# Kernel tuning notes

Hardware: AMD Instinct MI355X
Metric: run time of the kernel (lower is better)

Reference implementation:

```python
import jax, jax.numpy as jnp
import numpy as np

N = 50000      # nodes
E = 600000     # edges (avg degree 12)
F_IN = 128     # num_features
H = 128        # hidden_feats (== F_IN so both conv layers share weight shapes)
C = 10         # num_classes
L = 2          # num_layers


def setup_inputs() -> dict:
    key = jax.random.key(0)
    ks = jax.random.split(key, 12)
    s = 0.05
    x = jax.random.normal(ks[0], (N, F_IN), dtype=jnp.float32)
    edge_index = jax.random.randint(ks[1], (2, E), 0, N, dtype=jnp.int64)
    # Stacked per-layer TransformerConv params (heads=1): query/key/value/skip linears.
    Wq = jax.random.normal(ks[2], (L, H, F_IN), dtype=jnp.float32) * s
    bq = jax.random.normal(ks[3], (L, H), dtype=jnp.float32) * s
    Wk = jax.random.normal(ks[4], (L, H, F_IN), dtype=jnp.float32) * s
    bk = jax.random.normal(ks[5], (L, H), dtype=jnp.float32) * s
    Wv = jax.random.normal(ks[6], (L, H, F_IN), dtype=jnp.float32) * s
    bv = jax.random.normal(ks[7], (L, H), dtype=jnp.float32) * s
    Ws = jax.random.normal(ks[8], (L, H, F_IN), dtype=jnp.float32) * s
    bs = jax.random.normal(ks[9], (L, H), dtype=jnp.float32) * s
    fc_W = jax.random.normal(ks[10], (C, H), dtype=jnp.float32) * s
    fc_b = jax.random.normal(ks[11], (C,), dtype=jnp.float32) * s
    return {"x": x, "edge_index": edge_index, "Wq": Wq, "bq": bq, "Wk": Wk,
            "bk": bk, "Wv": Wv, "bv": bv, "Ws": Ws, "bs": bs,
            "fc_W": fc_W, "fc_b": fc_b}


def _transformer_conv(h, src, dst, Wq, bq, Wk, bk, Wv, bv, Ws, bs):
    # PyG TransformerConv, heads=1, concat=True, root_weight=True, eval mode.
    d = Wq.shape[0]
    scale = 1.0 / np.sqrt(d).astype(np.float32)
    q = h @ Wq.T + bq          # [N, d]
    k = h @ Wk.T + bk          # [N, d]
    v = h @ Wv.T + bv          # [N, d]
    # per-edge attention score: <q_dst, k_src> / sqrt(d)
    scores = jnp.sum(q[dst] * k[src], axis=-1) * scale   # [E]
    # scatter-softmax over incoming edges of each destination node
    m = jax.ops.segment_max(scores, dst, num_segments=N)           # [N]
    e = jnp.exp(scores - m[dst])                                   # [E]
    denom = jax.ops.segment_sum(e, dst, num_segments=N)            # [N]
    alpha = e / denom[dst]                                         # [E]
    agg = jax.ops.segment_sum(alpha[:, None] * v[src], dst, num_segments=N)  # [N, d]
    return agg + (h @ Ws.T + bs)  # root/skip connection


def reference(x, edge_index, Wq, bq, Wk, bk, Wv, bv, Ws, bs, fc_W, fc_b):
    src = edge_index[0]
    dst = edge_index[1]
    h = x
    for l in range(L):  # fixed small layer loop
        h = _transformer_conv(h, src, dst, Wq[l], bq[l], Wk[l], bk[l],
                              Wv[l], bv[l], Ws[l], bs[l])
        h = jax.nn.relu(h)  # dropout is identity in eval mode
    logits = h @ fc_W.T + fc_b  # [N, C]
    return jax.nn.log_softmax(logits, axis=1)
```

## Files before the change

### kernel.cpp

```cpp
#include <hip/hip_runtime.h>
#include <math.h>

#define N_NODES 50000
#define N_EDGES 600000
#define DIM 128
#define NCLS 10
#define MTILES 391
#define CHUNKS_PER_TILE 2048
#define NB_SCAN 49

typedef _Float16 h2 __attribute__((ext_vector_type(2)));
typedef _Float16 half8 __attribute__((ext_vector_type(8)));
typedef __attribute__((ext_vector_type(4))) float f32x4;
typedef unsigned char uchar;

__device__ inline h2 pkh(float a, float b) {
    auto r = __builtin_amdgcn_cvt_pkrtz(a, b);
    return *(h2*)&r;
}
__device__ inline unsigned h2u(h2 v) { return *(unsigned*)&v; }
__device__ inline h2 u2h(unsigned u) { return *(h2*)&u; }

__device__ inline float dot2acc(h2 a, h2 b, float c) {
#if __has_builtin(__builtin_amdgcn_fdot2)
    return __builtin_amdgcn_fdot2(a, b, c, false);
#else
    return fmaf((float)a.x, (float)b.x, fmaf((float)a.y, (float)b.y, c));
#endif
}

__device__ inline h2 dec2lo(unsigned w) {
    return u2h(__builtin_amdgcn_perm(0u, w, 0x010C000Cu));
}
__device__ inline h2 dec2hi(unsigned w) {
    return u2h(__builtin_amdgcn_perm(0u, w, 0x030C020Cu));
}
__device__ inline unsigned rnd8(h2 v) {
    unsigned u = h2u(v);
    return u + 0x007F007Fu + ((u >> 8) & 0x00010001u);
}

__global__ void deg_kernel(const int* __restrict__ dst, int* __restrict__ deg) {
    int e = blockIdx.x * blockDim.x + threadIdx.x;
    if (e < N_EDGES) atomicAdd(&deg[dst[e]], 1);
}

__global__ __launch_bounds__(1024) void scan1_kernel(
        const int* __restrict__ deg, int* __restrict__ row_start,
        int* __restrict__ partials) {
    __shared__ int buf[1024];
    int b = blockIdx.x, t = threadIdx.x;
    int i = b * 1024 + t;
    buf[t] = (i < N_NODES) ? deg[i] : 0;
    __syncthreads();
    for (int off = 1; off < 1024; off <<= 1) {
        int tv = (t >= off) ? buf[t - off] : 0;
        __syncthreads();
        buf[t] += tv;
        __syncthreads();
    }
    if (i < N_NODES) row_start[i + 1] = buf[t];
    if (t == 1023) partials[b] = buf[1023];
}

__global__ __launch_bounds__(1024) void scan3_kernel(
        const int* __restrict__ partials, int* __restrict__ row_start,
        int* __restrict__ cursor, int* __restrict__ col) {
    __shared__ int boff_s;
    int b = blockIdx.x, t = threadIdx.x;
    if (t < 64) {
        int v = (t < b) ? partials[t] : 0;
        #pragma unroll
        for (int off = 32; off >= 1; off >>= 1) v += __shfl_xor(v, off);
        if (t == 0) boff_s = v;
    }
    __syncthreads();
    int boff = boff_s;
    int i = b * 1024 + t;
    if (i < N_NODES) {
        int val = row_start[i + 1] + boff;
        row_start[i + 1] = val;
        if (i + 1 < N_NODES) cursor[i + 1] = val;
    }
    if (i == 0) { row_start[0] = 0; cursor[0] = 0; }
    if (b == 0 && t < 16) col[N_EDGES + t] = 0;
}

__global__ void fill_kernel(const int* __restrict__ src, const int* __restrict__ dst,
                            int* __restrict__ cursor, int* __restrict__ col) {
    int e = blockIdx.x * blockDim.x + threadIdx.x;
    if (e < N_EDGES) {
        int pos = atomicAdd(&cursor[dst[e]], 1);
        col[pos] = src[e];
    }
}

__global__ __launch_bounds__(256) void convertw_kernel(
        const float* __restrict__ Wq, const float* __restrict__ Wk,
        const float* __restrict__ Wv, const float* __restrict__ Ws,
        unsigned short* __restrict__ wfrag) {
    int b = blockIdx.x;
    int l = b >> 2, m = b & 3;
    const float* W = (m == 0 ? Wq : m == 1 ? Wk : m == 2 ? Wv : Ws) + l * DIM * DIM;
    unsigned short* out = wfrag + (size_t)b * (CHUNKS_PER_TILE * 8);
    for (int i = threadIdx.x; i < CHUNKS_PER_TILE; i += 256) {
        int tile = i >> 6, lane = i & 63;
        int row = (tile >> 2) * 16 + (lane & 15);
        int k0 = (tile & 3) * 32 + (lane >> 4) * 8;
        const float4* p = (const float4*)(W + row * DIM + k0);
        float4 a = p[0], bb = p[1];
        uint4 o;
        o.x = h2u(pkh(a.x, a.y));  o.y = h2u(pkh(a.z, a.w));
        o.z = h2u(pkh(bb.x, bb.y)); o.w = h2u(pkh(bb.z, bb.w));
        *(uint4*)(out + (size_t)i * 8) = o;
    }
}

template <bool F32IN>
__global__ __launch_bounds__(512) void linear_kernel(
        const void* __restrict__ hb_,
        const unsigned short* __restrict__ wfrag,
        const float* __restrict__ bq, const float* __restrict__ bk,
        const float* __restrict__ bv, const float* __restrict__ bs,
        unsigned short* __restrict__ Qb, uchar* __restrict__ K8,
        uchar* __restrict__ V8, unsigned short* __restrict__ Sb) {
    __shared__ unsigned short hs[16384];
    __shared__ unsigned short wsm[16384];
    int tid = threadIdx.x;
    int tile = blockIdx.x;
    uint4* lh = (uint4*)hs;
    uint4* lw = (uint4*)wsm;
    #pragma unroll
    for (int j = 0; j < 4; ++j) {
        int i = tid + j * 512;
        int s = i >> 6, lane = i & 63;
        int row = tile * 128 + ((s >> 2) << 4) + (lane & 15);
        int k0 = ((s & 3) << 5) + ((lane >> 4) << 3);
        row = row < N_NODES ? row : N_NODES - 1;
        if (F32IN) {
            const float* hf = (const float*)hb_;
            const float4* p = (const float4*)(hf + (size_t)row * DIM + k0);
            float4 a = p[0], bb = p[1];
            uint4 o;
            o.x = h2u(pkh(a.x, a.y));  o.y = h2u(pkh(a.z, a.w));
            o.z = h2u(pkh(bb.x, bb.y)); o.w = h2u(pkh(bb.z, bb.w));
            lh[i] = o;
        } else {
            const unsigned short* hh = (const unsigned short*)hb_;
            lh[i] = *(const uint4*)(hh + (size_t)row * DIM + k0);
        }
    }
    int wave = tid >> 6, lane = tid & 63;
    int node = tile * 128 + wave * 16 + (lane & 15);
    int cq = (lane >> 4) * 4;

    #pragma unroll
    for (int m = 0; m < 4; ++m) {
        const uint4* gw = (const uint4*)(wfrag + (size_t)m * (CHUNKS_PER_TILE * 8));
        __syncthreads();
        #pragma unroll
        for (int j = 0; j < 4; ++j) lw[tid + j * 512] = gw[tid + j * 512];
        __syncthreads();

        f32x4 acc[8];
        #pragma unroll
        for (int nt = 0; nt < 8; ++nt) acc[nt] = (f32x4){0.f, 0.f, 0.f, 0.f};
        #pragma unroll
        for (int ks = 0; ks < 4; ++ks) {
            half8 hbv = *(const half8*)(lh + (wave * 4 + ks) * 64 + lane);
            #pragma unroll
            for (int nt = 0; nt < 8; ++nt)
                acc[nt] = __builtin_amdgcn_mfma_f32_16x16x32_f16(
                              *(const half8*)(lw + (nt * 4 + ks) * 64 + lane),
                              hbv, acc[nt], 0, 0, 0);
        }

        const float* bias = (m == 0 ? bq : m == 1 ? bk : m == 2 ? bv : bs);
        if (node < N_NODES) {
            if (m == 0 || m == 3) {
                unsigned short* ob = (m == 0) ? Qb : Sb;
                #pragma unroll
                for (int nt = 0; nt < 8; ++nt) {
                    int colv = nt * 16 + cq;
                    float4 bi = *(const float4*)(bias + colv);
                    uint2 o;
                    o.x = h2u(pkh(acc[nt][0] + bi.x, acc[nt][1] + bi.y));
                    o.y = h2u(pkh(acc[nt][2] + bi.z, acc[nt][3] + bi.w));
                    *(uint2*)(ob + (size_t)node * DIM + colv) = o;
                }
            } else {
                uchar* ob = ((m == 1) ? K8 : V8) + (size_t)node * DIM;
                #pragma unroll
                for (int nt = 0; nt < 8; ++nt) {
                    int colv = nt * 16 + cq;
                    float4 bi = *(const float4*)(bias + colv);
                    unsigned uA = rnd8(pkh(acc[nt][0] + bi.x, acc[nt][1] + bi.y));
                    unsigned uB = rnd8(pkh(acc[nt][2] + bi.z, acc[nt][3] + bi.w));
                    *(unsigned*)(ob + colv) =
                        __builtin_amdgcn_perm(uB, uA, 0x07050301u);
                }
            }
        }
    }
}

template <bool LOGITS>
__global__ __launch_bounds__(256, 4) void attn_kernel(
        const unsigned short* __restrict__ Qb, const uchar* __restrict__ K8,
        const uchar* __restrict__ V8, const unsigned short* __restrict__ Sb,
        const int* __restrict__ row_start, const int* __restrict__ col,
        unsigned short* __restrict__ hout, float* __restrict__ outF,
        const float* __restrict__ fcW, const float* __restrict__ fcb) {
    int wave = threadIdx.x >> 6;
    int lane = threadIdx.x & 63;
    int g = lane >> 4, gl = lane & 15;
    int n = blockIdx.x * 4 + wave;
    if (n >= N_NODES) return;

    const uchar* Kc = K8 + (gl << 3);
    const uchar* Vc = V8 + (gl << 3);
    const float qsf = 0.08838834764831843f * 1.4426950408889634f;
    h2 qsv = pkh(qsf, qsf);
    uint4 qu = *(const uint4*)((const char*)Qb + (((unsigned)n) << 8) + (gl << 4));
    h2 q0 = u2h(qu.x) * qsv, q1 = u2h(qu.y) * qsv;
    h2 q2 = u2h(qu.z) * qsv, q3 = u2h(qu.w) * qsv;

    int e0 = row_start[n], e1 = row_start[n + 1];
    int deg = e1 - e0;
    const float NEG = -1.0e30f;
    float den = 0.f;
    h2 a0 = (h2)0, a1 = (h2)0, a2 = (h2)0, a3 = (h2)0;

#define LOAD4(eb_, k_, v_)                                                  \
    do {                                                                     \
        unsigned o0 = ((unsigned)col[(eb_)]) << 7;                           \
        unsigned o1 = ((unsigned)col[(eb_) + 4]) << 7;                       \
        unsigned o2 = ((unsigned)col[(eb_) + 8]) << 7;                       \
        unsigned o3 = ((unsigned)col[(eb_) + 12]) << 7;                      \
        k_[0] = *(const uint2*)(Kc + o0); v_[0] = *(const uint2*)(Vc + o0);  \
        k_[1] = *(const uint2*)(Kc + o1); v_[1] = *(const uint2*)(Vc + o1);  \
        k_[2] = *(const uint2*)(Kc + o2); v_[2] = *(const uint2*)(Vc + o2);  \
        k_[3] = *(const uint2*)(Kc + o3); v_[3] = *(const uint2*)(Vc + o3);  \
    } while (0)

#define EDOT(ku_) ({                                                         \
        float p_ = dot2acc(dec2lo((ku_).x), q0, 0.f);                        \
        p_ = dot2acc(dec2hi((ku_).x), q1, p_);                               \
        p_ = dot2acc(dec2lo((ku_).y), q2, p_);                               \
        p_ = dot2acc(dec2hi((ku_).y), q3, p_);                               \
        p_ += __shfl_xor(p_, 1); p_ += __shfl_xor(p_, 2);                    \
        p_ += __shfl_xor(p_, 4); p_ += __shfl_xor(p_, 8);                    \
        p_; })

#define ACCE(w_, vu_)                                                        \
    do {                                                                     \
        h2 w2 = pkh(w_, w_);                                                 \
        a0 = a0 + w2 * dec2lo((vu_).x);                                      \
        a1 = a1 + w2 * dec2hi((vu_).x);                                      \
        a2 = a2 + w2 * dec2lo((vu_).y);                                      \
        a3 = a3 + w2 * dec2hi((vu_).y);                                      \
    } while (0)

#define COMPUTE4(eb_, k_, v_)                                                \
    do {                                                                     \
        float p0 = EDOT(k_[0]), p1 = EDOT(k_[1]);                            \
        float p2 = EDOT(k_[2]), p3 = EDOT(k_[3]);                            \
        p0 = (eb_) < e1      ? p0 : NEG;                                     \
        p1 = (eb_) + 4 < e1  ? p1 : NEG;                                     \
        p2 = (eb_) + 8 < e1  ? p2 : NEG;                                     \
        p3 = (eb_) + 12 < e1 ? p3 : NEG;                                     \
        float w0 = exp2f(p0), w1 = exp2f(p1);                                \
        float w2_ = exp2f(p2), w3 = exp2f(p3);                               \
        den += (w0 + w1) + (w2_ + w3);                                       \
        ACCE(w0, v_[0]); ACCE(w1, v_[1]);                                    \
        ACCE(w2_, v_[2]); ACCE(w3, v_[3]);                                   \
    } while (0)

    if (deg > 0) {
        int B = (deg + 15) >> 4;
        int eb = e0 + g;
        uint2 k[4], v[4];
        LOAD4(eb, k, v);
        for (int b = 0;;) {
            uint2 nk[4], nv[4];
            bool more = (b + 1 < B);
            if (more) LOAD4(eb + 16, nk, nv);
            COMPUTE4(eb, k, v);
            if (!more) break;
            ++b; eb += 16;
            #pragma unroll
            for (int i = 0; i < 4; ++i) { k[i] = nk[i]; v[i] = nv[i]; }
        }
    }
#undef LOAD4
#undef EDOT
#undef ACCE
#undef COMPUTE4

    float d = den;
    d += __shfl_xor(d, 16);
    d += __shfl_xor(d, 32);
    a0 = a0 + u2h((unsigned)__shfl_xor((int)h2u(a0), 16));
    a0 = a0 + u2h((unsigned)__shfl_xor((int)h2u(a0), 32));
    a1 = a1 + u2h((unsigned)__shfl_xor((int)h2u(a1), 16));
    a1 = a1 + u2h((unsigned)__shfl_xor((int)h2u(a1), 32));
    a2 = a2 + u2h((unsigned)__shfl_xor((int)h2u(a2), 16));
    a2 = a2 + u2h((unsigned)__shfl_xor((int)h2u(a2), 32));
    a3 = a3 + u2h((unsigned)__shfl_xor((int)h2u(a3), 16));
    a3 = a3 + u2h((unsigned)__shfl_xor((int)h2u(a3), 32));
    float inv = (d > 0.f) ? 1.f / d : 0.f;

    uint4 su = *(const uint4*)((const char*)Sb + (((unsigned)n) << 8) + (gl << 4));
    h2 s0 = u2h(su.x), s1 = u2h(su.y), s2 = u2h(su.z), s3 = u2h(su.w);
    float o0 = fmaxf(fmaf((float)a0.x, inv, (float)s0.x), 0.f);
    float o1 = fmaxf(fmaf((float)a0.y, inv, (float)s0.y), 0.f);
    float o2 = fmaxf(fmaf((float)a1.x, inv, (float)s1.x), 0.f);
    float o3 = fmaxf(fmaf((float)a1.y, inv, (float)s1.y), 0.f);
    float o4 = fmaxf(fmaf((float)a2.x, inv, (float)s2.x), 0.f);
    float o5 = fmaxf(fmaf((float)a2.y, inv, (float)s2.y), 0.f);
    float o6 = fmaxf(fmaf((float)a3.x, inv, (float)s3.x), 0.f);
    float o7 = fmaxf(fmaf((float)a3.y, inv, (float)s3.y), 0.f);

    if (!LOGITS) {
        if (g == 0) {
            uint4 o;
            o.x = h2u(pkh(o0, o1)); o.y = h2u(pkh(o2, o3));
            o.z = h2u(pkh(o4, o5)); o.w = h2u(pkh(o6, o7));
            *(uint4*)((char*)hout + (((unsigned)n) << 8) + (gl << 4)) = o;
        }
    } else {
        float lg[NCLS];
        #pragma unroll
        for (int c = 0; c < NCLS; ++c) {
            const float4* fw = (const float4*)(fcW + c * DIM + gl * 8);
            float4 wa = fw[0], wb = fw[1];
            float pc = o0 * wa.x + o1 * wa.y + o2 * wa.z + o3 * wa.w
                     + o4 * wb.x + o5 * wb.y + o6 * wb.z + o7 * wb.w;
            pc += __shfl_xor(pc, 1); pc += __shfl_xor(pc, 2);
            pc += __shfl_xor(pc, 4); pc += __shfl_xor(pc, 8);
            lg[c] = pc + fcb[c];
        }
        float mx = lg[0];
        #pragma unroll
        for (int c = 1; c < NCLS; ++c) mx = fmaxf(mx, lg[c]);
        float se = 0.f;
        #pragma unroll
        for (int c = 0; c < NCLS; ++c) se += __expf(lg[c] - mx);
        float lse = mx + logf(se);
        if (g == 0 && gl < NCLS) {
            float myv = 0.f;
            #pragma unroll
            for (int c = 0; c < NCLS; ++c) if (gl == c) myv = lg[c];
            outF[(size_t)n * NCLS + gl] = myv - lse;
        }
    }
}

extern "C" void kernel_launch(void* const* d_in, const int* in_sizes, int n_in,
                              void* d_out, int out_size, void* d_ws, size_t ws_size,
                              hipStream_t stream) {
    const float* x   = (const float*)d_in[0];
    const int*   ei  = (const int*)d_in[1];
    const float* Wq  = (const float*)d_in[2];
    const float* bq  = (const float*)d_in[3];
    const float* Wk  = (const float*)d_in[4];
    const float* bk  = (const float*)d_in[5];
    const float* Wv  = (const float*)d_in[6];
    const float* bv  = (const float*)d_in[7];
    const float* Ws  = (const float*)d_in[8];
    const float* bs  = (const float*)d_in[9];
    const float* fcW = (const float*)d_in[10];
    const float* fcb = (const float*)d_in[11];
    const int* src = ei;
    const int* dst = ei + N_EDGES;

    size_t NF = (size_t)N_NODES * DIM;
    unsigned short* Qb = (unsigned short*)d_ws;
    unsigned short* Sb = Qb + NF;
    uchar* K8 = (uchar*)(Sb + NF);
    uchar* V8 = K8 + NF;
    unsigned short* h1 = (unsigned short*)(V8 + NF);
    unsigned short* wfrag = h1 + NF;
    int* ints      = (int*)(wfrag + 8 * CHUNKS_PER_TILE * 8);
    int* row_start = ints;
    int* cursor    = row_start + N_NODES + 1;
    int* col       = cursor + N_NODES;
    int* partials  = col + N_EDGES + 16;

    (void)hipMemsetAsync(cursor, 0, N_NODES * sizeof(int), stream);
    deg_kernel<<<(N_EDGES + 255) / 256, 256, 0, stream>>>(dst, cursor);
    scan1_kernel<<<NB_SCAN, 1024, 0, stream>>>(cursor, row_start, partials);
    scan3_kernel<<<NB_SCAN, 1024, 0, stream>>>(partials, row_start, cursor, col);
    fill_kernel<<<(N_EDGES + 255) / 256, 256, 0, stream>>>(src, dst, cursor, col);

    convertw_kernel<<<8, 256, 0, stream>>>(Wq, Wk, Wv, Ws, wfrag);

    const int AGRID = (N_NODES + 3) / 4;

    linear_kernel<true><<<MTILES, 512, 0, stream>>>(x, wfrag, bq, bk, bv, bs,
                                                    Qb, K8, V8, Sb);
    attn_kernel<false><<<AGRID, 256, 0, stream>>>(Qb, K8, V8, Sb, row_start, col,
                                                  h1, nullptr, nullptr, nullptr);
    linear_kernel<false><<<MTILES, 512, 0, stream>>>(h1, wfrag + 4 * CHUNKS_PER_TILE * 8,
                                                     bq + DIM, bk + DIM, bv + DIM, bs + DIM,
                                                     Qb, K8, V8, Sb);
    attn_kernel<true><<<AGRID, 256, 0, stream>>>(Qb, K8, V8, Sb, row_start, col,
                                                 nullptr, (float*)d_out, fcW, fcb);
}
```

Measured before the change: 228.6 us.

## Store K/V as fp16 instead of fp8, simplify attention loop, prefetch weights

Result: slower. 273.2 us (+19.5%).

```diff
diff --git a/kernel.cpp b/kernel.cpp
--- a/kernel.cpp
+++ b/kernel.cpp
@@ -27,17 +27,6 @@
 #else
     return fmaf((float)a.x, (float)b.x, fmaf((float)a.y, (float)b.y, c));
 #endif
-}
-
-__device__ inline h2 dec2lo(unsigned w) {
-    return u2h(__builtin_amdgcn_perm(0u, w, 0x010C000Cu));
-}
-__device__ inline h2 dec2hi(unsigned w) {
-    return u2h(__builtin_amdgcn_perm(0u, w, 0x030C020Cu));
-}
-__device__ inline unsigned rnd8(h2 v) {
-    unsigned u = h2u(v);
-    return u + 0x007F007Fu + ((u >> 8) & 0x00010001u);
 }
 
 __global__ void deg_kernel(const int* __restrict__ dst, int* __restrict__ deg) {
@@ -122,8 +111,8 @@
         const unsigned short* __restrict__ wfrag,
         const float* __restrict__ bq, const float* __restrict__ bk,
         const float* __restrict__ bv, const float* __restrict__ bs,
-        unsigned short* __restrict__ Qb, uchar* __restrict__ K8,
-        uchar* __restrict__ V8, unsigned short* __restrict__ Sb) {
+        unsigned short* __restrict__ Qb, unsigned short* __restrict__ K16,
+        unsigned short* __restrict__ V16, unsigned short* __restrict__ Sb) {
     __shared__ unsigned short hs[16384];
     __shared__ unsigned short wsm[16384];
     int tid = threadIdx.x;
@@ -154,13 +143,22 @@
     int node = tile * 128 + wave * 16 + (lane & 15);
     int cq = (lane >> 4) * 4;
 
+    uint4 wreg[4];
+    #pragma unroll
+    for (int j = 0; j < 4; ++j)
+        wreg[j] = ((const uint4*)wfrag)[tid + j * 512];
+
     #pragma unroll
     for (int m = 0; m < 4; ++m) {
-        const uint4* gw = (const uint4*)(wfrag + (size_t)m * (CHUNKS_PER_TILE * 8));
         __syncthreads();
         #pragma unroll
-        for (int j = 0; j < 4; ++j) lw[tid + j * 512] = gw[tid + j * 512];
+        for (int j = 0; j < 4; ++j) lw[tid + j * 512] = wreg[j];
         __syncthreads();
+        if (m < 3) {
+            const uint4* gw = (const uint4*)(wfrag + (size_t)(m + 1) * (CHUNKS_PER_TILE * 8));
+            #pragma unroll
+            for (int j = 0; j < 4; ++j) wreg[j] = gw[tid + j * 512];
+        }
 
         f32x4 acc[8];
         #pragma unroll
@@ -176,38 +174,25 @@
         }
 
         const float* bias = (m == 0 ? bq : m == 1 ? bk : m == 2 ? bv : bs);
+        unsigned short* ob = (m == 0 ? Qb : m == 1 ? K16 : m == 2 ? V16 : Sb);
         if (node < N_NODES) {
-            if (m == 0 || m == 3) {
-                unsigned short* ob = (m == 0) ? Qb : Sb;
-                #pragma unroll
-                for (int nt = 0; nt < 8; ++nt) {
-                    int colv = nt * 16 + cq;
-                    float4 bi = *(const float4*)(bias + colv);
-                    uint2 o;
-                    o.x = h2u(pkh(acc[nt][0] + bi.x, acc[nt][1] + bi.y));
-                    o.y = h2u(pkh(acc[nt][2] + bi.z, acc[nt][3] + bi.w));
-                    *(uint2*)(ob + (size_t)node * DIM + colv) = o;
-                }
-            } else {
-                uchar* ob = ((m == 1) ? K8 : V8) + (size_t)node * DIM;
-                #pragma unroll
-                for (int nt = 0; nt < 8; ++nt) {
-                    int colv = nt * 16 + cq;
-                    float4 bi = *(const float4*)(bias + colv);
-                    unsigned uA = rnd8(pkh(acc[nt][0] + bi.x, acc[nt][1] + bi.y));
-                    unsigned uB = rnd8(pkh(acc[nt][2] + bi.z, acc[nt][3] + bi.w));
-                    *(unsigned*)(ob + colv) =
-                        __builtin_amdgcn_perm(uB, uA, 0x07050301u);
-                }
+            #pragma unroll
+            for (int nt = 0; nt < 8; ++nt) {
+                int colv = nt * 16 + cq;
+                float4 bi = *(const float4*)(bias + colv);
+                uint2 o;
+                o.x = h2u(pkh(acc[nt][0] + bi.x, acc[nt][1] + bi.y));
+                o.y = h2u(pkh(acc[nt][2] + bi.z, acc[nt][3] + bi.w));
+                *(uint2*)(ob + (size_t)node * DIM + colv) = o;
             }
         }
     }
 }
 
 template <bool LOGITS>
-__global__ __launch_bounds__(256, 4) void attn_kernel(
-        const unsigned short* __restrict__ Qb, const uchar* __restrict__ K8,
-        const uchar* __restrict__ V8, const unsigned short* __restrict__ Sb,
+__global__ __launch_bounds__(256) void attn_kernel(
+        const unsigned short* __restrict__ Qb, const unsigned short* __restrict__ K16,
+        const unsigned short* __restrict__ V16, const unsigned short* __restrict__ Sb,
         const int* __restrict__ row_start, const int* __restrict__ col,
         unsigned short* __restrict__ hout, float* __restrict__ outF,
         const float* __restrict__ fcW, const float* __restrict__ fcb) {
@@ -217,85 +202,38 @@
     int n = blockIdx.x * 4 + wave;
     if (n >= N_NODES) return;
 
-    const uchar* Kc = K8 + (gl << 3);
-    const uchar* Vc = V8 + (gl << 3);
+    const uchar* Kc = (const uchar*)K16 + (gl << 4);
+    const uchar* Vc = (const uchar*)V16 + (gl << 4);
     const float qsf = 0.08838834764831843f * 1.4426950408889634f;
     h2 qsv = pkh(qsf, qsf);
-    uint4 qu = *(const uint4*)((const char*)Qb + (((unsigned)n) << 8) + (gl << 4));
+    uint4 qu = *(const uint4*)((const uchar*)Qb + (((unsigned)n) << 8) + (gl << 4));
     h2 q0 = u2h(qu.x) * qsv, q1 = u2h(qu.y) * qsv;
     h2 q2 = u2h(qu.z) * qsv, q3 = u2h(qu.w) * qsv;
 
     int e0 = row_start[n], e1 = row_start[n + 1];
-    int deg = e1 - e0;
-    const float NEG = -1.0e30f;
     float den = 0.f;
     h2 a0 = (h2)0, a1 = (h2)0, a2 = (h2)0, a3 = (h2)0;
 
-#define LOAD4(eb_, k_, v_)                                                  \
-    do {                                                                     \
-        unsigned o0 = ((unsigned)col[(eb_)]) << 7;                           \
-        unsigned o1 = ((unsigned)col[(eb_) + 4]) << 7;                       \
-        unsigned o2 = ((unsigned)col[(eb_) + 8]) << 7;                       \
-        unsigned o3 = ((unsigned)col[(eb_) + 12]) << 7;                      \
-        k_[0] = *(const uint2*)(Kc + o0); v_[0] = *(const uint2*)(Vc + o0);  \
-        k_[1] = *(const uint2*)(Kc + o1); v_[1] = *(const uint2*)(Vc + o1);  \
-        k_[2] = *(const uint2*)(Kc + o2); v_[2] = *(const uint2*)(Vc + o2);  \
-        k_[3] = *(const uint2*)(Kc + o3); v_[3] = *(const uint2*)(Vc + o3);  \
-    } while (0)
-
-#define EDOT(ku_) ({                                                         \
-        float p_ = dot2acc(dec2lo((ku_).x), q0, 0.f);                        \
-        p_ = dot2acc(dec2hi((ku_).x), q1, p_);                               \
-        p_ = dot2acc(dec2lo((ku_).y), q2, p_);                               \
-        p_ = dot2acc(dec2hi((ku_).y), q3, p_);                               \
-        p_ += __shfl_xor(p_, 1); p_ += __shfl_xor(p_, 2);                    \
-        p_ += __shfl_xor(p_, 4); p_ += __shfl_xor(p_, 8);                    \
-        p_; })
-
-#define ACCE(w_, vu_)                                                        \
-    do {                                                                     \
-        h2 w2 = pkh(w_, w_);                                                 \
-        a0 = a0 + w2 * dec2lo((vu_).x);                                      \
-        a1 = a1 + w2 * dec2hi((vu_).x);                                      \
-        a2 = a2 + w2 * dec2lo((vu_).y);                                      \
-        a3 = a3 + w2 * dec2hi((vu_).y);                                      \
-    } while (0)
-
-#define COMPUTE4(eb_, k_, v_)                                                \
-    do {                                                                     \
-        float p0 = EDOT(k_[0]), p1 = EDOT(k_[1]);                            \
-        float p2 = EDOT(k_[2]), p3 = EDOT(k_[3]);                            \
-        p0 = (eb_) < e1      ? p0 : NEG;                                     \
-        p1 = (eb_) + 4 < e1  ? p1 : NEG;                                     \
-        p2 = (eb_) + 8 < e1  ? p2 : NEG;                                     \
-        p3 = (eb_) + 12 < e1 ? p3 : NEG;                                     \
-        float w0 = exp2f(p0), w1 = exp2f(p1);                                \
-        float w2_ = exp2f(p2), w3 = exp2f(p3);                               \
-        den += (w0 + w1) + (w2_ + w3);                                       \
-        ACCE(w0, v_[0]); ACCE(w1, v_[1]);                                    \
-        ACCE(w2_, v_[2]); ACCE(w3, v_[3]);                                   \
-    } while (0)
-
-    if (deg > 0) {
-        int B = (deg + 15) >> 4;
-        int eb = e0 + g;
-        uint2 k[4], v[4];
-        LOAD4(eb, k, v);
-        for (int b = 0;;) {
-            uint2 nk[4], nv[4];
-            bool more = (b + 1 < B);
-            if (more) LOAD4(eb + 16, nk, nv);
-            COMPUTE4(eb, k, v);
-            if (!more) break;
-            ++b; eb += 16;
-            #pragma unroll
-            for (int i = 0; i < 4; ++i) { k[i] = nk[i]; v[i] = nv[i]; }
-        }
-    }
-#undef LOAD4
-#undef EDOT
-#undef ACCE
-#undef COMPUTE4
+    for (int e = e0 + g; e < e1; e += 4) {
+        unsigned off = ((unsigned)col[e]) << 8;
+        uint4 kv = *(const uint4*)(Kc + off);
+        uint4 vv = *(const uint4*)(Vc + off);
+        float p = dot2acc(u2h(kv.x), q0, 0.f);
+        p = dot2acc(u2h(kv.y), q1, p);
+        p = dot2acc(u2h(kv.z), q2, p);
+        p = dot2acc(u2h(kv.w), q3, p);
+        p += __shfl_xor(p, 1);
+        p += __shfl_xor(p, 2);
+        p += __shfl_xor(p, 4);
+        p += __shfl_xor(p, 8);
+        float w = exp2f(p);
+        den += w;
+        h2 w2 = pkh(w, w);
+        a0 = a0 + w2 * u2h(vv.x);
+        a1 = a1 + w2 * u2h(vv.y);
+        a2 = a2 + w2 * u2h(vv.z);
+        a3 = a3 + w2 * u2h(vv.w);
+    }
 
     float d = den;
     d += __shfl_xor(d, 16);
@@ -310,7 +248,7 @@
     a3 = a3 + u2h((unsigned)__shfl_xor((int)h2u(a3), 32));
     float inv = (d > 0.f) ? 1.f / d : 0.f;
 
-    uint4 su = *(const uint4*)((const char*)Sb + (((unsigned)n) << 8) + (gl << 4));
+    uint4 su = *(const uint4*)((const uchar*)Sb + (((unsigned)n) << 8) + (gl << 4));
     h2 s0 = u2h(su.x), s1 = u2h(su.y), s2 = u2h(su.z), s3 = u2h(su.w);
     float o0 = fmaxf(fmaf((float)a0.x, inv, (float)s0.x), 0.f);
     float o1 = fmaxf(fmaf((float)a0.y, inv, (float)s0.y), 0.f);
@@ -326,7 +264,7 @@
             uint4 o;
             o.x = h2u(pkh(o0, o1)); o.y = h2u(pkh(o2, o3));
             o.z = h2u(pkh(o4, o5)); o.w = h2u(pkh(o6, o7));
-            *(uint4*)((char*)hout + (((unsigned)n) << 8) + (gl << 4)) = o;
+            *(uint4*)((uchar*)hout + (((unsigned)n) << 8) + (gl << 4)) = o;
         }
     } else {
         float lg[NCLS];
@@ -375,11 +313,11 @@
     const int* dst = ei + N_EDGES;
 
     size_t NF = (size_t)N_NODES * DIM;
-    unsigned short* Qb = (unsigned short*)d_ws;
-    unsigned short* Sb = Qb + NF;
-    uchar* K8 = (uchar*)(Sb + NF);
-    uchar* V8 = K8 + NF;
-    unsigned short* h1 = (unsigned short*)(V8 + NF);
+    unsigned short* Qb  = (unsigned short*)d_ws;
+    unsigned short* Sb  = Qb + NF;
+    unsigned short* K16 = Sb + NF;
+    unsigned short* V16 = K16 + NF;
+    unsigned short* h1  = V16 + NF;
     unsigned short* wfrag = h1 + NF;
     int* ints      = (int*)(wfrag + 8 * CHUNKS_PER_TILE * 8);
     int* row_start = ints;
@@ -398,12 +336,12 @@
     const int AGRID = (N_NODES + 3) / 4;
 
     linear_kernel<true><<<MTILES, 512, 0, stream>>>(x, wfrag, bq, bk, bv, bs,
-                                                    Qb, K8, V8, Sb);
-    attn_kernel<false><<<AGRID, 256, 0, stream>>>(Qb, K8, V8, Sb, row_start, col,
+                                                    Qb, K16, V16, Sb);
+    attn_kernel<false><<<AGRID, 256, 0, stream>>>(Qb, K16, V16, Sb, row_start, col,
                                                   h1, nullptr, nullptr, nullptr);
     linear_kernel<false><<<MTILES, 512, 0, stream>>>(h1, wfrag + 4 * CHUNKS_PER_TILE * 8,
                                                      bq + DIM, bk + DIM, bv + DIM, bs + DIM,
-                                                     Qb, K8, V8, Sb);
-    attn_kernel<true><<<AGRID, 256, 0, stream>>>(Qb, K8, V8, Sb, row_start, col,
+                                                     Qb, K16, V16, Sb);
+    attn_kernel<true><<<AGRID, 256, 0, stream>>>(Qb, K16, V16, Sb, row_start, col,
                                                  nullptr, (float*)d_out, fcW, fcb);
 }
```

## Schedule attention waves by node degree via bucketed permutation

Applied to the files above, without the earlier changes.

After: 550.5 us. 141% more time.

```diff
diff --git a/kernel.cpp b/kernel.cpp
--- a/kernel.cpp
+++ b/kernel.cpp
@@ -92,6 +92,36 @@
     if (e < N_EDGES) {
         int pos = atomicAdd(&cursor[dst[e]], 1);
         col[pos] = src[e];
+    }
+}
+
+__global__ void bucket_kernel(const int* __restrict__ row_start, int* __restrict__ bcnt) {
+    int n = blockIdx.x * 256 + threadIdx.x;
+    if (n < N_NODES) {
+        int d = row_start[n + 1] - row_start[n];
+        d = d > 63 ? 63 : d;
+        atomicAdd(&bcnt[63 - d], 1);
+    }
+}
+__global__ void bscan_kernel(const int* __restrict__ bcnt, int* __restrict__ bcur) {
+    int l = threadIdx.x;
+    int v = bcnt[l];
+    int inc = v;
+    #pragma unroll
+    for (int off = 1; off < 64; off <<= 1) {
+        int t = __shfl_up(inc, off);
+        if (l >= off) inc += t;
+    }
+    bcur[l] = inc - v;
+}
+__global__ void scatter_kernel(const int* __restrict__ row_start,
+                               int* __restrict__ bcur, int* __restrict__ perm) {
+    int n = blockIdx.x * 256 + threadIdx.x;
+    if (n < N_NODES) {
+        int d = row_start[n + 1] - row_start[n];
+        d = d > 63 ? 63 : d;
+        int pos = atomicAdd(&bcur[63 - d], 1);
+        perm[pos] = n;
     }
 }
 
@@ -209,19 +239,19 @@
         const unsigned short* __restrict__ Qb, const uchar* __restrict__ K8,
         const uchar* __restrict__ V8, const unsigned short* __restrict__ Sb,
         const int* __restrict__ row_start, const int* __restrict__ col,
+        const int* __restrict__ perm,
         unsigned short* __restrict__ hout, float* __restrict__ outF,
         const float* __restrict__ fcW, const float* __restrict__ fcb) {
     int wave = threadIdx.x >> 6;
     int lane = threadIdx.x & 63;
     int g = lane >> 4, gl = lane & 15;
-    int n = blockIdx.x * 4 + wave;
-    if (n >= N_NODES) return;
+    int n = perm[(blockIdx.x << 2) + wave];
 
     const uchar* Kc = K8 + (gl << 3);
     const uchar* Vc = V8 + (gl << 3);
     const float qsf = 0.08838834764831843f * 1.4426950408889634f;
     h2 qsv = pkh(qsf, qsf);
-    uint4 qu = *(const uint4*)((const char*)Qb + (((unsigned)n) << 8) + (gl << 4));
+    uint4 qu = *(const uint4*)((const uchar*)Qb + (((unsigned)n) << 8) + (gl << 4));
     h2 q0 = u2h(qu.x) * qsv, q1 = u2h(qu.y) * qsv;
     h2 q2 = u2h(qu.z) * qsv, q3 = u2h(qu.w) * qsv;
 
@@ -310,7 +340,7 @@
     a3 = a3 + u2h((unsigned)__shfl_xor((int)h2u(a3), 32));
     float inv = (d > 0.f) ? 1.f / d : 0.f;
 
-    uint4 su = *(const uint4*)((const char*)Sb + (((unsigned)n) << 8) + (gl << 4));
+    uint4 su = *(const uint4*)((const uchar*)Sb + (((unsigned)n) << 8) + (gl << 4));
     h2 s0 = u2h(su.x), s1 = u2h(su.y), s2 = u2h(su.z), s3 = u2h(su.w);
     float o0 = fmaxf(fmaf((float)a0.x, inv, (float)s0.x), 0.f);
     float o1 = fmaxf(fmaf((float)a0.y, inv, (float)s0.y), 0.f);
@@ -326,7 +356,7 @@
             uint4 o;
             o.x = h2u(pkh(o0, o1)); o.y = h2u(pkh(o2, o3));
             o.z = h2u(pkh(o4, o5)); o.w = h2u(pkh(o6, o7));
-            *(uint4*)((char*)hout + (((unsigned)n) << 8) + (gl << 4)) = o;
+            *(uint4*)((uchar*)hout + (((unsigned)n) << 8) + (gl << 4)) = o;
         }
     } else {
         float lg[NCLS];
@@ -384,26 +414,33 @@
     int* ints      = (int*)(wfrag + 8 * CHUNKS_PER_TILE * 8);
     int* row_start = ints;
     int* cursor    = row_start + N_NODES + 1;
-    int* col       = cursor + N_NODES;
+    int* bcnt      = cursor + N_NODES;
+    int* bcur      = bcnt + 64;
+    int* col       = bcur + 64;
     int* partials  = col + N_EDGES + 16;
-
-    (void)hipMemsetAsync(cursor, 0, N_NODES * sizeof(int), stream);
+    int* perm      = partials + 64;
+
+    (void)hipMemsetAsync(cursor, 0, (N_NODES + 128) * sizeof(int), stream);
     deg_kernel<<<(N_EDGES + 255) / 256, 256, 0, stream>>>(dst, cursor);
     scan1_kernel<<<NB_SCAN, 1024, 0, stream>>>(cursor, row_start, partials);
     scan3_kernel<<<NB_SCAN, 1024, 0, stream>>>(partials, row_start, cursor, col);
     fill_kernel<<<(N_EDGES + 255) / 256, 256, 0, stream>>>(src, dst, cursor, col);
 
+    bucket_kernel<<<(N_NODES + 255) / 256, 256, 0, stream>>>(row_start, bcnt);
+    bscan_kernel<<<1, 64, 0, stream>>>(bcnt, bcur);
+    scatter_kernel<<<(N_NODES + 255) / 256, 256, 0, stream>>>(row_start, bcur, perm);
+
     convertw_kernel<<<8, 256, 0, stream>>>(Wq, Wk, Wv, Ws, wfrag);
 
-    const int AGRID = (N_NODES + 3) / 4;
+    const int AGRID = N_NODES / 4;
 
     linear_kernel<true><<<MTILES, 512, 0, stream>>>(x, wfrag, bq, bk, bv, bs,
                                                     Qb, K8, V8, Sb);
     attn_kernel<false><<<AGRID, 256, 0, stream>>>(Qb, K8, V8, Sb, row_start, col,
-                                                  h1, nullptr, nullptr, nullptr);
+                                                  perm, h1, nullptr, nullptr, nullptr);
     linear_kernel<false><<<MTILES, 512, 0, stream>>>(h1, wfrag + 4 * CHUNKS_PER_TILE * 8,
                                                      bq + DIM, bk + DIM, bv + DIM, bs + DIM,
                                                      Qb, K8, V8, Sb);
     attn_kernel<true><<<AGRID, 256, 0, stream>>>(Qb, K8, V8, Sb, row_start, col,
-                                                 nullptr, (float*)d_out, fcW, fcb);
-}
+                                                 perm, nullptr, (float*)d_out, fcW, fcb);
+}
```
